# Optimization experiments

Measured on AMD Instinct MI355X. Metric: run time of the kernel, lower is better.

The kernel has to match this reference:

```python
import jax, jax.numpy as jnp
import numpy as np

B, NQ, NK, D = 64, 1024, 1024, 128
MASK_VALUE = -1e6


def setup_inputs() -> dict:
    key = jax.random.key(0)
    kq, kk, kv, kl = jax.random.split(key, 4)
    queries = jax.random.normal(kq, (B, NQ, D), dtype=jnp.float32)
    keys = jax.random.normal(kk, (B, NK, D), dtype=jnp.float32)
    values = jax.random.normal(kv, (B, NK, D), dtype=jnp.float32)
    valid_lens = jax.random.randint(kl, (B,), 1, NK + 1, dtype=jnp.int32)
    return {"queries": queries, "keys": keys, "values": values, "valid_lens": valid_lens}


def reference(queries, keys, values, valid_lens):
    d = queries.shape[-1]
    # scores: [B, Nq, Nk]
    scores = jnp.einsum("bqd,bkd->bqk", queries, keys) / jnp.sqrt(jnp.float32(d))
    # valid_lens [B] -> mask over last (key) axis, same for every query row
    key_pos = jnp.arange(scores.shape[-1])  # [Nk]
    mask = key_pos[None, None, :] < valid_lens[:, None, None]  # [B,1,Nk] broadcast
    scores = jnp.where(mask, scores, jnp.float32(MASK_VALUE))
    attn = jax.nn.softmax(scores, axis=-1)
    # dropout p=0.0 (eval): identity
    return jnp.einsum("bqk,bkd->bqd", attn, values)
```

## Files before the change

### kernel.cpp

```cpp
#include <hip/hip_runtime.h>

typedef __bf16 bf16x8 __attribute__((ext_vector_type(8)));
typedef __bf16 bf16x2 __attribute__((ext_vector_type(2)));
typedef float f32x4 __attribute__((ext_vector_type(4)));
typedef int i32x4 __attribute__((ext_vector_type(4)));

namespace {
constexpr int kNQ = 1024;
constexpr int kNK = 1024;
constexpr int kD = 128;
constexpr int kBQ = 64;
constexpr int kBK = 32;
constexpr int kTileElems = 4096;
constexpr float kScaleLog2e = 0.12751742f;
}

__device__ __forceinline__ int packbf(float a, float b) {
    bf16x2 t; t[0] = (__bf16)a; t[1] = (__bf16)b;
    return __builtin_bit_cast(int, t);
}

__device__ __forceinline__ void async16(const __bf16* g, const __bf16* l) {
    __builtin_amdgcn_global_load_lds(
        (const __attribute__((address_space(1))) void*)g,
        (__attribute__((address_space(3))) void*)l, 16, 0, 0);
}

__global__ void lpt_sort(const int* __restrict__ VL, int* __restrict__ perm) {
    const int t = threadIdx.x;
    const int v = VL[t];
    int rank = 0;
    for (int j = 0; j < 64; ++j) {
        const int vj = VL[j];
        rank += (vj > v) || (vj == v && j < t);
    }
    perm[rank] = t;
}

__global__ void repack(const float* __restrict__ K, const float* __restrict__ V,
                       const int* __restrict__ VL,
                       __bf16* __restrict__ Kimg, __bf16* __restrict__ Vimg) {
    const int blk = blockIdx.x;
    const int b = blk >> 5, t = blk & 31;
    if (t * kBK >= VL[b]) return;
    const int tid = threadIdx.x;
    __shared__ float vbuf[32 * 132];

    const size_t tileofs = (size_t)(b * 32 + t) * kTileElems;

    #pragma unroll
    for (int it = 0; it < 2; ++it) {
        const int chunk = tid + it * 256;
        const int k = chunk >> 4;
        const int p = chunk & 15;
        const int c = p ^ (k & 15);
        const float* src = K + (((size_t)b * kNK + t * kBK + k) * kD + c * 8);
        const f32x4 x0 = *(const f32x4*)src;
        const f32x4 x1 = *(const f32x4*)(src + 4);
        bf16x8 h;
        #pragma unroll
        for (int j = 0; j < 4; ++j) { h[j] = (__bf16)x0[j]; h[4 + j] = (__bf16)x1[j]; }
        *(bf16x8*)(Kimg + tileofs + chunk * 8) = h;
    }

    {
        const int r = tid >> 3, col0 = (tid & 7) * 16;
        const float* src = V + (((size_t)b * kNK + t * kBK + r) * kD + col0);
        #pragma unroll
        for (int j = 0; j < 4; ++j) {
            const f32x4 x = *(const f32x4*)(src + j * 4);
            *(f32x4*)&vbuf[r * 132 + col0 + j * 4] = x;
        }
    }
    __syncthreads();
    #pragma unroll
    for (int it = 0; it < 2; ++it) {
        const int chunk = tid + it * 256;
        const int d = chunk >> 2;
        const int p = chunk & 3;
        const int q = p ^ ((d >> 1) & 3);
        bf16x8 h;
        #pragma unroll
        for (int j = 0; j < 8; ++j) h[j] = (__bf16)vbuf[(q * 8 + j) * 132 + d];
        *(bf16x8*)(Vimg + tileofs + chunk * 8) = h;
    }
}

__global__ __launch_bounds__(128)
void fa_fwd(const float* __restrict__ Q, const int* __restrict__ VL,
            const int* __restrict__ perm, const __bf16* __restrict__ Kimg,
            const __bf16* __restrict__ Vimg, float* __restrict__ O)
{
    __shared__ __align__(16) __bf16 kls[2][kTileElems];
    __shared__ __align__(16) __bf16 vls[2][kTileElems];

    const int tid  = threadIdx.x;
    const int wave = tid >> 6;
    const int lane = tid & 63;
    const int quad = lane >> 4;
    const int c16  = lane & 15;

    const int i = blockIdx.x;
    const int g = i >> 8;
    const int j = i & 255;
    int rank;
    if      (g == 0) rank = j;
    else if (g == 1) rank = 511 - j;
    else if (g == 2) rank = 512 + j;
    else             rank = 1023 - j;

    const int b    = perm[rank >> 4];
    const int qblk = rank & 15;
    const int q0   = qblk * kBQ + wave * 32;

    const int valid  = VL[b];
    const int ntiles = (valid + kBK - 1) / kBK;
    const size_t bT  = (size_t)b * 32;

    bf16x8 qf[2][4];
    #pragma unroll
    for (int gg = 0; gg < 2; ++gg) {
        const float* qp = Q + ((size_t)b * kNQ + q0 + gg * 16 + c16) * kD + quad * 8;
        #pragma unroll
        for (int f = 0; f < 4; ++f) {
            #pragma unroll
            for (int jj = 0; jj < 8; ++jj) qf[gg][f][jj] = (__bf16)qp[f * 32 + jj];
        }
    }

    bf16x8 ones;
    #pragma unroll
    for (int jj = 0; jj < 8; ++jj) ones[jj] = (__bf16)1.0f;

    f32x4 acc[2][9];
    #pragma unroll
    for (int gg = 0; gg < 2; ++gg)
        #pragma unroll
        for (int f = 0; f < 9; ++f) {
            acc[gg][f][0] = 0.f; acc[gg][f][1] = 0.f;
            acc[gg][f][2] = 0.f; acc[gg][f][3] = 0.f;
        }

    auto stage = [&](int bufi, int t) {
        const __bf16* kg = Kimg + (bT + t) * kTileElems;
        const __bf16* vg = Vimg + (bT + t) * kTileElems;
        #pragma unroll
        for (int ii = 0; ii < 4; ++ii) {
            const int seg = (wave * 4 + ii) * 512;
            async16(kg + seg + lane * 8, &kls[bufi][seg]);
            async16(vg + seg + lane * 8, &vls[bufi][seg]);
        }
    };

    const int a0 = ((quad & 1) << 7) + (c16 << 2);
    const int a1 = a0 + 64;
    const bool lo = quad < 2;

    auto cToA = [&](const f32x4& sA, const f32x4& sB) -> bf16x8 {
        const int p01 = packbf(sA[0], sA[1]), p23 = packbf(sA[2], sA[3]);
        const int q01 = packbf(sB[0], sB[1]), q23 = packbf(sB[2], sB[3]);
        const int b0p = __builtin_amdgcn_ds_bpermute(a0, p01);
        const int b0q = __builtin_amdgcn_ds_bpermute(a0, q01);
        const int b1p = __builtin_amdgcn_ds_bpermute(a0, p23);
        const int b1q = __builtin_amdgcn_ds_bpermute(a0, q23);
        const int b2p = __builtin_amdgcn_ds_bpermute(a1, p01);
        const int b2q = __builtin_amdgcn_ds_bpermute(a1, q01);
        const int b3p = __builtin_amdgcn_ds_bpermute(a1, p23);
        const int b3q = __builtin_amdgcn_ds_bpermute(a1, q23);
        i32x4 pd;
        pd[0] = lo ? b0p : b0q;
        pd[1] = lo ? b1p : b1q;
        pd[2] = lo ? b2p : b2q;
        pd[3] = lo ? b3p : b3q;
        return __builtin_bit_cast(bf16x8, pd);
    };

    const int vsw = (quad ^ ((c16 >> 1) & 3)) << 3;

    stage(0, 0);
    __syncthreads();

    for (int t = 0; t < ntiles; ++t) {
        const int cur = t & 1;
        if (t + 1 < ntiles) stage(cur ^ 1, t + 1);

        f32x4 s00 = {0.f,0.f,0.f,0.f}, s01 = {0.f,0.f,0.f,0.f};
        f32x4 s10 = {0.f,0.f,0.f,0.f}, s11 = {0.f,0.f,0.f,0.f};
        #pragma unroll
        for (int f = 0; f < 4; ++f) {
            const int perm4 = ((f * 4 + quad) ^ c16) << 3;
            const bf16x8 kf = *(const bf16x8*)&kls[cur][c16 * 128 + perm4];
            s00 = __builtin_amdgcn_mfma_f32_16x16x32_bf16(kf, qf[0][f], s00, 0, 0, 0);
            s01 = __builtin_amdgcn_mfma_f32_16x16x32_bf16(kf, qf[1][f], s01, 0, 0, 0);
        }
        #pragma unroll
        for (int f = 0; f < 4; ++f) {
            const int perm4 = ((f * 4 + quad) ^ c16) << 3;
            const bf16x8 kf = *(const bf16x8*)&kls[cur][(16 + c16) * 128 + perm4];
            s10 = __builtin_amdgcn_mfma_f32_16x16x32_bf16(kf, qf[0][f], s10, 0, 0, 0);
            s11 = __builtin_amdgcn_mfma_f32_16x16x32_bf16(kf, qf[1][f], s11, 0, 0, 0);
        }

        const int kb = t * kBK;
        if (kb + kBK > valid) {
            #pragma unroll
            for (int r = 0; r < 4; ++r) {
                if (kb + quad * 4 + r >= valid)      { s00[r] = -1e30f; s01[r] = -1e30f; }
                if (kb + 16 + quad * 4 + r >= valid) { s10[r] = -1e30f; s11[r] = -1e30f; }
            }
        }

        #pragma unroll
        for (int r = 0; r < 4; ++r) {
            s00[r] = __builtin_amdgcn_exp2f(s00[r] * kScaleLog2e);
            s01[r] = __builtin_amdgcn_exp2f(s01[r] * kScaleLog2e);
            s10[r] = __builtin_amdgcn_exp2f(s10[r] * kScaleLog2e);
            s11[r] = __builtin_amdgcn_exp2f(s11[r] * kScaleLog2e);
        }

        const bf16x8 pf0 = cToA(s00, s10);
        const bf16x8 pf1 = cToA(s01, s11);

        #pragma unroll
        for (int f = 0; f < 8; ++f) {
            const bf16x8 vf = *(const bf16x8*)&vls[cur][(f * 16 + c16) * 32 + vsw];
            acc[0][f] = __builtin_amdgcn_mfma_f32_16x16x32_bf16(pf0, vf, acc[0][f], 0, 0, 0);
            acc[1][f] = __builtin_amdgcn_mfma_f32_16x16x32_bf16(pf1, vf, acc[1][f], 0, 0, 0);
        }
        acc[0][8] = __builtin_amdgcn_mfma_f32_16x16x32_bf16(pf0, ones, acc[0][8], 0, 0, 0);
        acc[1][8] = __builtin_amdgcn_mfma_f32_16x16x32_bf16(pf1, ones, acc[1][8], 0, 0, 0);

        __syncthreads();
    }

    float* ob = O + ((size_t)b * kNQ + q0) * kD;
    #pragma unroll
    for (int gg = 0; gg < 2; ++gg) {
        #pragma unroll
        for (int r = 0; r < 4; ++r) {
            const float inv = 1.0f / acc[gg][8][r];
            #pragma unroll
            for (int f = 0; f < 8; ++f) {
                ob[(gg * 16 + quad * 4 + r) * kD + f * 16 + c16] = acc[gg][f][r] * inv;
            }
        }
    }
}

extern "C" void kernel_launch(void* const* d_in, const int* in_sizes, int n_in,
                              void* d_out, int out_size, void* d_ws, size_t ws_size,
                              hipStream_t stream) {
    const float* Q = (const float*)d_in[0];
    const float* K = (const float*)d_in[1];
    const float* V = (const float*)d_in[2];
    const int*  VL = (const int*)d_in[3];
    float* O = (float*)d_out;

    int* perm = (int*)d_ws;
    __bf16* Kimg = (__bf16*)((char*)d_ws + 4096);
    __bf16* Vimg = (__bf16*)((char*)d_ws + 4096 + (size_t)16 * 1024 * 1024);

    lpt_sort<<<1, 64, 0, stream>>>(VL, perm);
    repack<<<dim3(64 * 32), 256, 0, stream>>>(K, V, VL, Kimg, Vimg);
    fa_fwd<<<dim3(1024), 128, 0, stream>>>(Q, VL, perm, Kimg, Vimg, O);
}
```

Before: 177.8 us.

## Use four waves per block, each owning 16 query rows

Raises the block size from 128 to 256 threads so each of four waves handles 16 query rows instead of two waves handling 32. The per-wave accumulator and Q-fragment register footprint is halved, and the QK^T chain is split into two independent MFMA accumulators to shorten dependency chains. This aims to raise wave-level parallelism and latency hiding per CU. In exchange, each K/V tile in LDS is reused by more waves, and each wave pays the bpermute transpose and loop overhead for half the MFMA work.

Result: faster. 172.3 us (-3.1%).

```diff
diff --git a/kernel.cpp b/kernel.cpp
--- a/kernel.cpp
+++ b/kernel.cpp
@@ -86,7 +86,7 @@
     }
 }
 
-__global__ __launch_bounds__(128)
+__global__ __launch_bounds__(256)
 void fa_fwd(const float* __restrict__ Q, const int* __restrict__ VL,
             const int* __restrict__ perm, const __bf16* __restrict__ Kimg,
             const __bf16* __restrict__ Vimg, float* __restrict__ O)
@@ -111,20 +111,19 @@
 
     const int b    = perm[rank >> 4];
     const int qblk = rank & 15;
-    const int q0   = qblk * kBQ + wave * 32;
+    const int q0   = qblk * kBQ + wave * 16;
 
     const int valid  = VL[b];
     const int ntiles = (valid + kBK - 1) / kBK;
     const size_t bT  = (size_t)b * 32;
 
-    bf16x8 qf[2][4];
-    #pragma unroll
-    for (int gg = 0; gg < 2; ++gg) {
-        const float* qp = Q + ((size_t)b * kNQ + q0 + gg * 16 + c16) * kD + quad * 8;
+    bf16x8 qf[4];
+    {
+        const float* qp = Q + ((size_t)b * kNQ + q0 + c16) * kD + quad * 8;
         #pragma unroll
         for (int f = 0; f < 4; ++f) {
             #pragma unroll
-            for (int jj = 0; jj < 8; ++jj) qf[gg][f][jj] = (__bf16)qp[f * 32 + jj];
+            for (int jj = 0; jj < 8; ++jj) qf[f][jj] = (__bf16)qp[f * 32 + jj];
         }
     }
 
@@ -132,21 +131,18 @@
     #pragma unroll
     for (int jj = 0; jj < 8; ++jj) ones[jj] = (__bf16)1.0f;
 
-    f32x4 acc[2][9];
-    #pragma unroll
-    for (int gg = 0; gg < 2; ++gg)
-        #pragma unroll
-        for (int f = 0; f < 9; ++f) {
-            acc[gg][f][0] = 0.f; acc[gg][f][1] = 0.f;
-            acc[gg][f][2] = 0.f; acc[gg][f][3] = 0.f;
-        }
+    f32x4 acc[9];
+    #pragma unroll
+    for (int f = 0; f < 9; ++f) {
+        acc[f][0] = 0.f; acc[f][1] = 0.f; acc[f][2] = 0.f; acc[f][3] = 0.f;
+    }
 
     auto stage = [&](int bufi, int t) {
         const __bf16* kg = Kimg + (bT + t) * kTileElems;
         const __bf16* vg = Vimg + (bT + t) * kTileElems;
         #pragma unroll
-        for (int ii = 0; ii < 4; ++ii) {
-            const int seg = (wave * 4 + ii) * 512;
+        for (int ii = 0; ii < 2; ++ii) {
+            const int seg = (wave * 2 + ii) * 512;
             async16(kg + seg + lane * 8, &kls[bufi][seg]);
             async16(vg + seg + lane * 8, &vls[bufi][seg]);
         }
@@ -156,93 +152,91 @@
     const int a1 = a0 + 64;
     const bool lo = quad < 2;
 
-    auto cToA = [&](const f32x4& sA, const f32x4& sB) -> bf16x8 {
-        const int p01 = packbf(sA[0], sA[1]), p23 = packbf(sA[2], sA[3]);
-        const int q01 = packbf(sB[0], sB[1]), q23 = packbf(sB[2], sB[3]);
-        const int b0p = __builtin_amdgcn_ds_bpermute(a0, p01);
-        const int b0q = __builtin_amdgcn_ds_bpermute(a0, q01);
-        const int b1p = __builtin_amdgcn_ds_bpermute(a0, p23);
-        const int b1q = __builtin_amdgcn_ds_bpermute(a0, q23);
-        const int b2p = __builtin_amdgcn_ds_bpermute(a1, p01);
-        const int b2q = __builtin_amdgcn_ds_bpermute(a1, q01);
-        const int b3p = __builtin_amdgcn_ds_bpermute(a1, p23);
-        const int b3q = __builtin_amdgcn_ds_bpermute(a1, q23);
+    const int vsw = (quad ^ ((c16 >> 1) & 3)) << 3;
+
+    stage(0, 0);
+    __syncthreads();
+
+    for (int t = 0; t < ntiles; ++t) {
+        const int cur = t & 1;
+        if (t + 1 < ntiles) stage(cur ^ 1, t + 1);
+
+        f32x4 s0a = {0.f,0.f,0.f,0.f}, s0b = {0.f,0.f,0.f,0.f};
+        f32x4 s1a = {0.f,0.f,0.f,0.f}, s1b = {0.f,0.f,0.f,0.f};
+        const __bf16* kbuf = kls[cur];
+        #pragma unroll
+        for (int f = 0; f < 2; ++f) {
+            const bf16x8 kf = *(const bf16x8*)&kbuf[c16 * 128 + (((f * 4 + quad) ^ c16) << 3)];
+            s0a = __builtin_amdgcn_mfma_f32_16x16x32_bf16(kf, qf[f], s0a, 0, 0, 0);
+        }
+        #pragma unroll
+        for (int f = 2; f < 4; ++f) {
+            const bf16x8 kf = *(const bf16x8*)&kbuf[c16 * 128 + (((f * 4 + quad) ^ c16) << 3)];
+            s0b = __builtin_amdgcn_mfma_f32_16x16x32_bf16(kf, qf[f], s0b, 0, 0, 0);
+        }
+        #pragma unroll
+        for (int f = 0; f < 2; ++f) {
+            const bf16x8 kf = *(const bf16x8*)&kbuf[(16 + c16) * 128 + (((f * 4 + quad) ^ c16) << 3)];
+            s1a = __builtin_amdgcn_mfma_f32_16x16x32_bf16(kf, qf[f], s1a, 0, 0, 0);
+        }
+        #pragma unroll
+        for (int f = 2; f < 4; ++f) {
+            const bf16x8 kf = *(const bf16x8*)&kbuf[(16 + c16) * 128 + (((f * 4 + quad) ^ c16) << 3)];
+            s1b = __builtin_amdgcn_mfma_f32_16x16x32_bf16(kf, qf[f], s1b, 0, 0, 0);
+        }
+        f32x4 s0 = s0a + s0b;
+        f32x4 s1 = s1a + s1b;
+
+        const int kb = t * kBK;
+        if (kb + kBK > valid) {
+            #pragma unroll
+            for (int r = 0; r < 4; ++r) {
+                if (kb + quad * 4 + r >= valid)      s0[r] = -1e30f;
+                if (kb + 16 + quad * 4 + r >= valid) s1[r] = -1e30f;
+            }
+        }
+
+        #pragma unroll
+        for (int r = 0; r < 4; ++r) {
+            s0[r] = __builtin_amdgcn_exp2f(s0[r] * kScaleLog2e);
+            s1[r] = __builtin_amdgcn_exp2f(s1[r] * kScaleLog2e);
+        }
+
+        const int pp01 = packbf(s0[0], s0[1]), pp23 = packbf(s0[2], s0[3]);
+        const int qq01 = packbf(s1[0], s1[1]), qq23 = packbf(s1[2], s1[3]);
+        const int b0p = __builtin_amdgcn_ds_bpermute(a0, pp01);
+        const int b0q = __builtin_amdgcn_ds_bpermute(a0, qq01);
+        const int b1p = __builtin_amdgcn_ds_bpermute(a0, pp23);
+        const int b1q = __builtin_amdgcn_ds_bpermute(a0, qq23);
+        const int b2p = __builtin_amdgcn_ds_bpermute(a1, pp01);
+        const int b2q = __builtin_amdgcn_ds_bpermute(a1, qq01);
+        const int b3p = __builtin_amdgcn_ds_bpermute(a1, pp23);
+        const int b3q = __builtin_amdgcn_ds_bpermute(a1, qq23);
         i32x4 pd;
         pd[0] = lo ? b0p : b0q;
         pd[1] = lo ? b1p : b1q;
         pd[2] = lo ? b2p : b2q;
         pd[3] = lo ? b3p : b3q;
-        return __builtin_bit_cast(bf16x8, pd);
-    };
-
-    const int vsw = (quad ^ ((c16 >> 1) & 3)) << 3;
-
-    stage(0, 0);
-    __syncthreads();
-
-    for (int t = 0; t < ntiles; ++t) {
-        const int cur = t & 1;
-        if (t + 1 < ntiles) stage(cur ^ 1, t + 1);
-
-        f32x4 s00 = {0.f,0.f,0.f,0.f}, s01 = {0.f,0.f,0.f,0.f};
-        f32x4 s10 = {0.f,0.f,0.f,0.f}, s11 = {0.f,0.f,0.f,0.f};
-        #pragma unroll
-        for (int f = 0; f < 4; ++f) {
-            const int perm4 = ((f * 4 + quad) ^ c16) << 3;
-            const bf16x8 kf = *(const bf16x8*)&kls[cur][c16 * 128 + perm4];
-            s00 = __builtin_amdgcn_mfma_f32_16x16x32_bf16(kf, qf[0][f], s00, 0, 0, 0);
-            s01 = __builtin_amdgcn_mfma_f32_16x16x32_bf16(kf, qf[1][f], s01, 0, 0, 0);
-        }
-        #pragma unroll
-        for (int f = 0; f < 4; ++f) {
-            const int perm4 = ((f * 4 + quad) ^ c16) << 3;
-            const bf16x8 kf = *(const bf16x8*)&kls[cur][(16 + c16) * 128 + perm4];
-            s10 = __builtin_amdgcn_mfma_f32_16x16x32_bf16(kf, qf[0][f], s10, 0, 0, 0);
-            s11 = __builtin_amdgcn_mfma_f32_16x16x32_bf16(kf, qf[1][f], s11, 0, 0, 0);
-        }
-
-        const int kb = t * kBK;
-        if (kb + kBK > valid) {
-            #pragma unroll
-            for (int r = 0; r < 4; ++r) {
-                if (kb + quad * 4 + r >= valid)      { s00[r] = -1e30f; s01[r] = -1e30f; }
-                if (kb + 16 + quad * 4 + r >= valid) { s10[r] = -1e30f; s11[r] = -1e30f; }
-            }
-        }
-
-        #pragma unroll
-        for (int r = 0; r < 4; ++r) {
-            s00[r] = __builtin_amdgcn_exp2f(s00[r] * kScaleLog2e);
-            s01[r] = __builtin_amdgcn_exp2f(s01[r] * kScaleLog2e);
-            s10[r] = __builtin_amdgcn_exp2f(s10[r] * kScaleLog2e);
-            s11[r] = __builtin_amdgcn_exp2f(s11[r] * kScaleLog2e);
-        }
-
-        const bf16x8 pf0 = cToA(s00, s10);
-        const bf16x8 pf1 = cToA(s01, s11);
-
+        const bf16x8 pf = __builtin_bit_cast(bf16x8, pd);
+
+        const __bf16* vbuf = vls[cur];
         #pragma unroll
         for (int f = 0; f < 8; ++f) {
-            const bf16x8 vf = *(const bf16x8*)&vls[cur][(f * 16 + c16) * 32 + vsw];
-            acc[0][f] = __builtin_amdgcn_mfma_f32_16x16x32_bf16(pf0, vf, acc[0][f], 0, 0, 0);
-            acc[1][f] = __builtin_amdgcn_mfma_f32_16x16x32_bf16(pf1, vf, acc[1][f], 0, 0, 0);
-        }
-        acc[0][8] = __builtin_amdgcn_mfma_f32_16x16x32_bf16(pf0, ones, acc[0][8], 0, 0, 0);
-        acc[1][8] = __builtin_amdgcn_mfma_f32_16x16x32_bf16(pf1, ones, acc[1][8], 0, 0, 0);
+            const bf16x8 vf = *(const bf16x8*)&vbuf[(f * 16 + c16) * 32 + vsw];
+            acc[f] = __builtin_amdgcn_mfma_f32_16x16x32_bf16(pf, vf, acc[f], 0, 0, 0);
+        }
+        acc[8] = __builtin_amdgcn_mfma_f32_16x16x32_bf16(pf, ones, acc[8], 0, 0, 0);
 
         __syncthreads();
     }
 
     float* ob = O + ((size_t)b * kNQ + q0) * kD;
     #pragma unroll
-    for (int gg = 0; gg < 2; ++gg) {
-        #pragma unroll
-        for (int r = 0; r < 4; ++r) {
-            const float inv = 1.0f / acc[gg][8][r];
-            #pragma unroll
-            for (int f = 0; f < 8; ++f) {
-                ob[(gg * 16 + quad * 4 + r) * kD + f * 16 + c16] = acc[gg][f][r] * inv;
-            }
+    for (int r = 0; r < 4; ++r) {
+        const float inv = 1.0f / acc[8][r];
+        #pragma unroll
+        for (int f = 0; f < 8; ++f) {
+            ob[(quad * 4 + r) * kD + f * 16 + c16] = acc[f][r] * inv;
         }
     }
 }
@@ -262,5 +256,5 @@
 
     lpt_sort<<<1, 64, 0, stream>>>(VL, perm);
     repack<<<dim3(64 * 32), 256, 0, stream>>>(K, V, VL, Kimg, Vimg);
-    fa_fwd<<<dim3(1024), 128, 0, stream>>>(Q, VL, perm, Kimg, Vimg, O);
-}
+    fa_fwd<<<dim3(1024), 256, 0, stream>>>(Q, VL, perm, Kimg, Vimg, O);
+}
```
